# Kernel tuning notes

Hardware: AMD Instinct MI355X
Metric: run time of the kernel (lower is better)

## Reference

```python
import jax, jax.numpy as jnp
import numpy as np

B = 32768
T = 30
H = 384


def setup_inputs() -> dict:
    key = jax.random.key(0)
    ks = jax.random.split(key, 16)

    def lin(k, out_d, in_d):
        # torch nn.Linear init: U(-1/sqrt(in_d), 1/sqrt(in_d))
        bound = 1.0 / np.sqrt(in_d)
        kw, kb = jax.random.split(k)
        W = jax.random.uniform(kw, (out_d, in_d), jnp.float32, -bound, bound)
        b = jax.random.uniform(kb, (out_d,), jnp.float32, -bound, bound)
        return W, b

    Wp, bp = lin(ks[0], 128, 3)        # plan_input
    Ws, bs = lin(ks[1], 128, 3)        # state_input
    # GRUCell params: weight_ih [3H,128], weight_hh [3H,H], init U(-1/sqrt(H),..)
    gb = 1.0 / np.sqrt(H)
    W_ih = jax.random.uniform(ks[2], (3 * H, 128), jnp.float32, -gb, gb)
    b_ih = jax.random.uniform(ks[3], (3 * H,), jnp.float32, -gb, gb)
    W_hh = jax.random.uniform(ks[4], (3 * H, H), jnp.float32, -gb, gb)
    b_hh = jax.random.uniform(ks[5], (3 * H,), jnp.float32, -gb, gb)
    Wd1, bd1 = lin(ks[6], 64, H)       # decode Linear(384,64)
    Wd2, bd2 = lin(ks[7], 3, 64)       # decode Linear(64,3)

    init_hidden = jax.random.normal(ks[8], (B, H), jnp.float32)
    plan = jax.random.normal(ks[9], (B, T, 3), jnp.float32)
    gate = jax.random.uniform(ks[10], (B, 1), jnp.float32)
    init_state = jax.random.normal(ks[11], (B, 3), jnp.float32)

    return {
        "init_hidden": init_hidden, "plan": plan, "gate": gate,
        "init_state": init_state,
        "Wp": Wp, "bp": bp, "Ws": Ws, "bs": bs,
        "W_ih": W_ih, "b_ih": b_ih, "W_hh": W_hh, "b_hh": b_hh,
        "Wd1": Wd1, "bd1": bd1, "Wd2": Wd2, "bd2": bd2,
    }


def reference(init_hidden, plan, gate, init_state,
              Wp, bp, Ws, bs, W_ih, b_ih, W_hh, b_hh,
              Wd1, bd1, Wd2, bd2):
    # Dropout(0.1) is identity in eval mode.
    plan_seq = jnp.swapaxes(plan[:, :T, :3], 0, 1)  # [T,B,3]

    def step(carry, plan_t):
        hidden, state = carry  # [B,H], [B,3]
        x = (state @ Ws.T + bs) + (plan_t @ Wp.T + bp) * gate  # [B,128]
        gi = x @ W_ih.T + b_ih          # [B,3H]
        gh = hidden @ W_hh.T + b_hh     # [B,3H]
        ir, iz, inn = jnp.split(gi, 3, axis=-1)
        hr, hz, hn = jnp.split(gh, 3, axis=-1)
        r = jax.nn.sigmoid(ir + hr)
        z = jax.nn.sigmoid(iz + hz)
        n = jnp.tanh(inn + r * hn)
        hidden = (1.0 - z) * n + z * hidden
        dec = jax.nn.elu(hidden @ Wd1.T + bd1) @ Wd2.T + bd2  # [B,3]
        state = dec + state
        return (hidden, state), state

    _, outs = jax.lax.scan(step, (init_hidden, init_state[:, :3]), plan_seq)
    return jnp.swapaxes(outs, 0, 1)  # [B,T,3]
```

## Files before the change

kernel.cpp:

```cpp
#include <hip/hip_runtime.h>


#define TT  30
#define NPH 50
#define PHU 12288
#define HPU 6144
#define STRU 614400
#define HS  392

typedef unsigned short u16;
typedef __bf16 bf16x8 __attribute__((ext_vector_type(8)));
typedef u16    u16x8  __attribute__((ext_vector_type(8)));
typedef float  f32x16 __attribute__((ext_vector_type(16)));

__device__ __forceinline__ u16 f2b(float f){
  unsigned u = __float_as_uint(f);
  u += 0x7FFFu + ((u >> 16) & 1u);
  return (u16)(u >> 16);
}
__device__ __forceinline__ float b2f(u16 h){ return __uint_as_float(((unsigned)h) << 16); }

__device__ __forceinline__ f32x16 mfma32(u16x8 a, u16x8 b, f32x16 c){
  return __builtin_amdgcn_mfma_f32_32x32x16_bf16(
      __builtin_bit_cast(bf16x8, a), __builtin_bit_cast(bf16x8, b), c, 0, 0, 0);
}
__device__ __forceinline__ void lds_fence(){
  asm volatile("s_waitcnt lgkmcnt(0)" ::: "memory");
  __builtin_amdgcn_sched_barrier(0);
}
__device__ __forceinline__ float sigf(float x){ return __builtin_amdgcn_rcpf(1.f + __expf(-x)); }
__device__ __forceinline__ float tanh_(float x){ return 2.f*__builtin_amdgcn_rcpf(1.f + __expf(-2.f*x)) - 1.f; }

__device__ __forceinline__ void stage16(const u16* g, u16* l){
  __builtin_amdgcn_global_load_lds(
      (const __attribute__((address_space(1))) unsigned int*)g,
      (__attribute__((address_space(3))) unsigned int*)l, 16, 0, 0);
}

__global__ void prep_kernel(const float* __restrict__ Wih, const float* __restrict__ Whh,
                            const float* __restrict__ Wd1, const float* __restrict__ Wd2,
                            const float* __restrict__ bih, const float* __restrict__ bhh,
                            const float* __restrict__ Ws,  const float* __restrict__ bs,
                            const float* __restrict__ Wp,  const float* __restrict__ bp,
                            u16* __restrict__ stream, u16* __restrict__ wd2p,
                            u16* __restrict__ wxp, float* __restrict__ gb)
{
  int i = blockIdx.x*blockDim.x + threadIdx.x;
  if (i < 442368){
    int row = i/384, k = i - row*384;
    int g = row/384, unit = row - g*384, c = unit>>5, lc = unit&31;
    int kf = k>>4, hl = (k>>3)&1, j = k&7;
    int phase = c*4 + 1 + g;
    stream[(size_t)phase*PHU + kf*512 + (lc+32*hl)*8 + j] = f2b(Whh[i]);
  }
  if (i < 147456){
    int row = i>>7, k = i&127;
    int g = row/384, unit = row - g*384, c = unit>>5, lc = unit&31;
    int kf = k>>4, hl = (k>>3)&1, j = k&7;
    int phase = c*4;
    stream[(size_t)phase*PHU + (g*8+kf)*512 + (lc+32*hl)*8 + j] = f2b(Wih[i]);
  }
  if (i < 24576){
    int row = i/384, k = i - row*384;
    int ct = row>>5, lc = row&31;
    int kf = k>>4, hl = (k>>3)&1, j = k&7;
    int phase = 48 + ct;
    stream[(size_t)phase*PHU + kf*512 + (lc+32*hl)*8 + j] = f2b(Wd1[i]);
  }
  if (i < 2048){
    int kf = i>>9, r = i&511;
    int n = (r>>3)&31, hl = r>>8, j = r&7;
    int k = kf*16 + hl*8 + j;
    wd2p[i] = f2b((n<3) ? Wd2[n*64 + k] : 0.f);
  }
  if (i < 2048){
    int tl = i>>9, r = i&511;
    int n = (r>>3)&31, hl = r>>8, j = r&7;
    int k = hl*8 + j, u = tl*32 + n;
    float v = 0.f;
    if      (k <= 2) v = Ws[u*3 + k];
    else if (k == 3) v = bs[u];
    else if (k <= 6) v = Wp[u*3 + (k-4)];
    else if (k == 7) v = bp[u];
    wxp[i] = f2b(v);
  }
  if (i < 384){
    gb[i*4+0] = bih[i]       + bhh[i];
    gb[i*4+1] = bih[384+i]   + bhh[384+i];
    gb[i*4+2] = bih[768+i];
    gb[i*4+3] = bhh[768+i];
  }
}

#define PRELOAD(BN) { \
  const u16* W0_ = wb + ra*HPU + lane*8; \
  const u16* W1_ = wb + rb*HPU + lane*8; \
  _Pragma("unroll") for (int f_=0; f_<12; ++f_) BN[f_]    = *(const u16x8*)(W0_ + f_*512); \
  _Pragma("unroll") for (int f_=0; f_<12; ++f_) BN[12+f_] = *(const u16x8*)(W1_ + f_*512); }

#define PH_GH(ACC, BC, BN) { \
  stage_half(); stage_half(); \
  PRELOAD(BN); \
  _Pragma("unroll") for (int kf_=0; kf_<24; ++kf_) ACC = mfma32(hold[kf_], BC[kf_], ACC); \
  phase_end(); }

#define PH_GI(BC, BN) { \
  stage_half(); stage_half(); \
  PRELOAD(BN); \
  _Pragma("unroll") for (int kf_=0; kf_<8; ++kf_){ \
    aR  = mfma32(xf[kf_], BC[kf_],    aR); \
    aZ  = mfma32(xf[kf_], BC[8+kf_],  aZ); \
    aNI = mfma32(xf[kf_], BC[16+kf_], aNI); } \
  phase_end(); }

__global__ __launch_bounds__(256, 1)
void gru_main(const float* __restrict__ ih, const float* __restrict__ plan,
              const float* __restrict__ gate, const float* __restrict__ istate,
              const u16* __restrict__ stream, const u16* __restrict__ wd2p,
              const u16* __restrict__ wxp, const float* __restrict__ gb,
              const float* __restrict__ bd1, const float* __restrict__ bd2,
              float* __restrict__ out)
{
  __shared__ __attribute__((aligned(16))) u16 wb[5*HPU];
  __shared__ __attribute__((aligned(16))) u16 hn[4][32*HS];

  const int tid  = threadIdx.x;
  const int wave = tid >> 6, lane = tid & 63;
  const int m    = lane & 31, hl = lane >> 5;
  const int R0   = blockIdx.x*128 + wave*32;
  u16* hw = hn[wave];

  const float gt    = gate[R0 + m];
  const float bd1v0 = bd1[m], bd1v1 = bd1[32+m];
  const float bd2v  = (m<3) ? bd2[m] : 0.f;

  if (lane < 32){
    const float* sp = istate + (size_t)(R0+lane)*3;
    float* q = (float*)&hw[lane*HS + 384];
    q[0]=sp[0]; q[1]=sp[1]; q[2]=sp[2]; q[3]=0.f;
  }

  u16x8 hold[24];
#pragma unroll
  for (int kf=0; kf<24; ++kf){
    const float* p = ih + (size_t)(R0+m)*384 + kf*16 + hl*8;
    float4 a = *(const float4*)p;
    float4 b = *(const float4*)(p+4);
    u16x8 v;
    v[0]=f2b(a.x); v[1]=f2b(a.y); v[2]=f2b(a.z); v[3]=f2b(a.w);
    v[4]=f2b(b.x); v[5]=f2b(b.y); v[6]=f2b(b.z); v[7]=f2b(b.w);
    hold[kf]=v;
    *(u16x8*)&hw[m*HS + kf*16 + hl*8] = v;
  }

  int hoff = 0;
  int ss   = 0;
  int ra   = 0, rb = 1;
  auto stage_half = [&](){
    const u16* s = stream + hoff + wave*1536 + lane*8;
    u16* d = &wb[ss*HPU + wave*1536];
    stage16(s,        d);
    stage16(s + 512,  d + 512);
    stage16(s + 1024, d + 1024);
    hoff += HPU; if (hoff == STRU) hoff = 0;
    ss = (ss==4) ? 0 : ss+1;
  };
  auto phase_end = [&](){
    asm volatile("s_waitcnt vmcnt(3) lgkmcnt(0)" ::: "memory");
    __builtin_amdgcn_sched_barrier(0);
    __builtin_amdgcn_s_barrier();
    __builtin_amdgcn_sched_barrier(0);
    ra = (ra>=3) ? ra-3 : ra+2;
    rb = (rb>=3) ? rb-3 : rb+2;
  };

  u16x8 bfA[24], bfB[24];

  stage_half(); stage_half();
  asm volatile("s_waitcnt vmcnt(0)" ::: "memory");
  __builtin_amdgcn_sched_barrier(0);
  __builtin_amdgcn_s_barrier();
  __builtin_amdgcn_sched_barrier(0);
  PRELOAD(bfA);
  stage_half(); stage_half(); stage_half();
  asm volatile("s_waitcnt vmcnt(3) lgkmcnt(0)" ::: "memory");
  __builtin_amdgcn_sched_barrier(0);
  __builtin_amdgcn_s_barrier();
  __builtin_amdgcn_sched_barrier(0);
  ra = 2; rb = 3;

#pragma unroll 1
  for (int t=0; t<TT; ++t){
    u16x8 a8;
    {
      float4 sv = *(const float4*)&hw[m*HS + 384];
      const float* pp = plan + (size_t)(R0+m)*(TT*3) + t*3;
      float f0=sv.x, f1=sv.y, f2=sv.z, f3=1.f;
      float f4=gt*pp[0], f5=gt*pp[1], f6=gt*pp[2], f7=gt;
      if (hl){ a8[0]=0;a8[1]=0;a8[2]=0;a8[3]=0;a8[4]=0;a8[5]=0;a8[6]=0;a8[7]=0; }
      else { a8[0]=f2b(f0);a8[1]=f2b(f1);a8[2]=f2b(f2);a8[3]=f2b(f3);
             a8[4]=f2b(f4);a8[5]=f2b(f5);a8[6]=f2b(f6);a8[7]=f2b(f7); }
    }
    u16x8 xf[8];
#pragma unroll
    for (int tl=0; tl<4; ++tl){
      f32x16 ax;
#pragma unroll
      for (int r=0;r<16;++r) ax[r]=0.f;
      ax = mfma32(a8, *(const u16x8*)(wxp + tl*512 + lane*8), ax);
#pragma unroll
      for (int r=0;r<16;++r){
        int row = (r&3) + ((r>>2)<<3) + 4*hl;
        hw[row*HS + m] = f2b(ax[r]);
      }
      lds_fence();
      xf[2*tl]   = *(const u16x8*)&hw[m*HS + hl*8];
      xf[2*tl+1] = *(const u16x8*)&hw[m*HS + 16 + hl*8];
      lds_fence();
    }
    *(u16x8*)&hw[m*HS + hl*8]      = hold[0];
    *(u16x8*)&hw[m*HS + 16 + hl*8] = hold[1];
    lds_fence();

#pragma unroll 1
    for (int c=0; c<12; ++c){
      f32x16 aR, aZ, aNI, aNH;
      {
        const float4 b4 = *(const float4*)(gb + (size_t)(c*32+m)*4);
#pragma unroll
        for (int r=0;r<16;++r){ aR[r]=b4.x; aZ[r]=b4.y; aNI[r]=b4.z; aNH[r]=b4.w; }
      }
      PH_GI(bfA, bfB);
      PH_GH(aR, bfB, bfA);
      PH_GH(aZ, bfA, bfB);
      {
        stage_half(); stage_half();
        PRELOAD(bfA);
#pragma unroll
        for (int kf=0; kf<24; ++kf)
          aNH = mfma32(hold[kf], bfB[kf], aNH);
#pragma unroll
        for (int r=0;r<16;++r){
          int row = (r&3) + ((r>>2)<<3) + 4*hl;
          float rr = sigf(aR[r]);
          float zz = sigf(aZ[r]);
          float nn = tanh_(aNI[r] + rr*aNH[r]);
          int off = row*HS + c*32 + m;
          float ho = b2f(hw[off]);
          hw[off] = f2b((1.f-zz)*nn + zz*ho);
        }
        phase_end();
      }
    }

    lds_fence();
#pragma unroll
    for (int kf=0; kf<24; ++kf)
      hold[kf] = *(const u16x8*)&hw[m*HS + kf*16 + hl*8];

    f32x16 a0, a1;
#pragma unroll
    for (int r=0;r<16;++r){ a0[r]=bd1v0; a1[r]=bd1v1; }
    PH_GH(a0, bfA, bfB);
    {
      stage_half(); stage_half();
      PRELOAD(bfA);
#pragma unroll
      for (int kf=0; kf<24; ++kf)
        a1 = mfma32(hold[kf], bfB[kf], a1);

      u16x8 wd2f0 = *(const u16x8*)(wd2p + 0*512 + lane*8);
      u16x8 wd2f1 = *(const u16x8*)(wd2p + 1*512 + lane*8);
      u16x8 wd2f2 = *(const u16x8*)(wd2p + 2*512 + lane*8);
      u16x8 wd2f3 = *(const u16x8*)(wd2p + 3*512 + lane*8);

      f32x16 ao;
#pragma unroll
      for (int r=0;r<16;++r) ao[r]=0.f;
#pragma unroll
      for (int r=0;r<16;++r){
        int row = (r&3) + ((r>>2)<<3) + 4*hl;
        float e = a0[r]; e = e>0.f ? e : (__expf(e)-1.f);
        hw[row*HS + m] = f2b(e);
      }
      lds_fence();
      {
        u16x8 af0 = *(const u16x8*)&hw[m*HS + hl*8];
        u16x8 af1 = *(const u16x8*)&hw[m*HS + 16 + hl*8];
        ao = mfma32(af0, wd2f0, ao);
        ao = mfma32(af1, wd2f1, ao);
      }
      lds_fence();
#pragma unroll
      for (int r=0;r<16;++r){
        int row = (r&3) + ((r>>2)<<3) + 4*hl;
        float e = a1[r]; e = e>0.f ? e : (__expf(e)-1.f);
        hw[row*HS + m] = f2b(e);
      }
      lds_fence();
      {
        u16x8 af0 = *(const u16x8*)&hw[m*HS + hl*8];
        u16x8 af1 = *(const u16x8*)&hw[m*HS + 16 + hl*8];
        ao = mfma32(af0, wd2f2, ao);
        ao = mfma32(af1, wd2f3, ao);
      }
      lds_fence();
      *(u16x8*)&hw[m*HS + hl*8]      = hold[0];
      *(u16x8*)&hw[m*HS + 16 + hl*8] = hold[1];

#pragma unroll
      for (int r=0;r<16;++r){
        int row = (r&3) + ((r>>2)<<3) + 4*hl;
        if (m < 3){
          float* q = (float*)&hw[row*HS + 384];
          float ns = q[m] + ao[r] + bd2v;
          out[(size_t)(R0+row)*(TT*3) + t*3 + m] = ns;
          q[m] = ns;
        }
      }
      phase_end();
    }
  }
}

extern "C" void kernel_launch(void* const* d_in, const int* in_sizes, int n_in,
                              void* d_out, int out_size, void* d_ws, size_t ws_size,
                              hipStream_t stream)
{
  (void)in_sizes; (void)n_in; (void)out_size; (void)ws_size;
  const float* ih     = (const float*)d_in[0];
  const float* plan   = (const float*)d_in[1];
  const float* gatep  = (const float*)d_in[2];
  const float* istate = (const float*)d_in[3];
  const float* Wp     = (const float*)d_in[4];
  const float* bp     = (const float*)d_in[5];
  const float* Ws     = (const float*)d_in[6];
  const float* bs     = (const float*)d_in[7];
  const float* Wih    = (const float*)d_in[8];
  const float* bih    = (const float*)d_in[9];
  const float* Whh    = (const float*)d_in[10];
  const float* bhh    = (const float*)d_in[11];
  const float* Wd1    = (const float*)d_in[12];
  const float* bd1    = (const float*)d_in[13];
  const float* Wd2    = (const float*)d_in[14];
  const float* bd2    = (const float*)d_in[15];

  u16*   wstream = (u16*)d_ws;
  u16*   wd2p    = (u16*)((char*)d_ws + 1228800);
  u16*   wxp     = (u16*)((char*)d_ws + 1232896);
  float* gb      = (float*)((char*)d_ws + 1236992);

  prep_kernel<<<1728, 256, 0, stream>>>(Wih, Whh, Wd1, Wd2, bih, bhh, Ws, bs, Wp, bp,
                                        wstream, wd2p, wxp, gb);
  gru_main<<<256, 256, 0, stream>>>(ih, plan, gatep, istate,
                                    wstream, wd2p, wxp, gb, bd1, bd2, (float*)d_out);
}
```

Measured before the change: 1.645 ms.

## Stream GRU weights directly from global/L2 into registers, dropping LDS staging

Replaces the cooperative global_load_lds staging of weight halves into a shared ring buffer, and its per-phase waitcnt and s_barrier, with per-wave direct global loads into register double buffers (bfA/bfB) that are issued in the middle of each phase's MFMA chain. The intent is to remove most block-wide barriers and the LDS round trip, so the four waves run independently and weight fetches overlap with compute. In exchange, every wave now fetches the full weight stream from L2 itself, which multiplies cache traffic by four. The prefetch distance is also only half a phase, so load latency may be exposed. One barrier per timestep is kept.

```diff
diff --git a/kernel.cpp b/kernel.cpp
--- a/kernel.cpp
+++ b/kernel.cpp
@@ -2,10 +2,8 @@
 
 
 #define TT  30
-#define NPH 50
 #define PHU 12288
 #define HPU 6144
-#define STRU 614400
 #define HS  392
 
 typedef unsigned short u16;
@@ -30,12 +28,6 @@
 }
 __device__ __forceinline__ float sigf(float x){ return __builtin_amdgcn_rcpf(1.f + __expf(-x)); }
 __device__ __forceinline__ float tanh_(float x){ return 2.f*__builtin_amdgcn_rcpf(1.f + __expf(-2.f*x)) - 1.f; }
-
-__device__ __forceinline__ void stage16(const u16* g, u16* l){
-  __builtin_amdgcn_global_load_lds(
-      (const __attribute__((address_space(1))) unsigned int*)g,
-      (__attribute__((address_space(3))) unsigned int*)l, 16, 0, 0);
-}
 
 __global__ void prep_kernel(const float* __restrict__ Wih, const float* __restrict__ Whh,
                             const float* __restrict__ Wd1, const float* __restrict__ Wd2,
@@ -92,26 +84,24 @@
   }
 }
 
-#define PRELOAD(BN) { \
-  const u16* W0_ = wb + ra*HPU + lane*8; \
-  const u16* W1_ = wb + rb*HPU + lane*8; \
-  _Pragma("unroll") for (int f_=0; f_<12; ++f_) BN[f_]    = *(const u16x8*)(W0_ + f_*512); \
-  _Pragma("unroll") for (int f_=0; f_<12; ++f_) BN[12+f_] = *(const u16x8*)(W1_ + f_*512); }
-
-#define PH_GH(ACC, BC, BN) { \
-  stage_half(); stage_half(); \
-  PRELOAD(BN); \
-  _Pragma("unroll") for (int kf_=0; kf_<24; ++kf_) ACC = mfma32(hold[kf_], BC[kf_], ACC); \
-  phase_end(); }
-
-#define PH_GI(BC, BN) { \
-  stage_half(); stage_half(); \
-  PRELOAD(BN); \
-  _Pragma("unroll") for (int kf_=0; kf_<8; ++kf_){ \
-    aR  = mfma32(xf[kf_], BC[kf_],    aR); \
-    aZ  = mfma32(xf[kf_], BC[8+kf_],  aZ); \
-    aNI = mfma32(xf[kf_], BC[16+kf_], aNI); } \
-  phase_end(); }
+#define LOAD_HALF(BN) { \
+  const u16* s_ = stream + (size_t)nh*HPU + lane*8; \
+  _Pragma("unroll") for (int f_=0; f_<12; ++f_) BN[f_] = *(const u16x8*)(s_ + f_*512); \
+  nh = (nh==99) ? 0 : nh+1; }
+
+#define PH_GI() { \
+  _Pragma("unroll") for (int q_=0;q_<8;++q_) aR  = mfma32(xf[q_],   bfA[q_],   aR); \
+  _Pragma("unroll") for (int q_=0;q_<4;++q_) aZ  = mfma32(xf[q_],   bfA[8+q_], aZ); \
+  LOAD_HALF(bfA); \
+  _Pragma("unroll") for (int q_=0;q_<4;++q_) aZ  = mfma32(xf[4+q_], bfB[q_],   aZ); \
+  _Pragma("unroll") for (int q_=0;q_<8;++q_) aNI = mfma32(xf[q_],   bfB[4+q_], aNI); \
+  LOAD_HALF(bfB); }
+
+#define PH_GH(ACC) { \
+  _Pragma("unroll") for (int k_=0;k_<12;++k_) ACC = mfma32(hold[k_],    bfA[k_], ACC); \
+  LOAD_HALF(bfA); \
+  _Pragma("unroll") for (int k_=0;k_<12;++k_) ACC = mfma32(hold[12+k_], bfB[k_], ACC); \
+  LOAD_HALF(bfB); }
 
 __global__ __launch_bounds__(256, 1)
 void gru_main(const float* __restrict__ ih, const float* __restrict__ plan,
@@ -121,7 +111,6 @@
               const float* __restrict__ bd1, const float* __restrict__ bd2,
               float* __restrict__ out)
 {
-  __shared__ __attribute__((aligned(16))) u16 wb[5*HPU];
   __shared__ __attribute__((aligned(16))) u16 hn[4][32*HS];
 
   const int tid  = threadIdx.x;
@@ -153,44 +142,15 @@
     *(u16x8*)&hw[m*HS + kf*16 + hl*8] = v;
   }
 
-  int hoff = 0;
-  int ss   = 0;
-  int ra   = 0, rb = 1;
-  auto stage_half = [&](){
-    const u16* s = stream + hoff + wave*1536 + lane*8;
-    u16* d = &wb[ss*HPU + wave*1536];
-    stage16(s,        d);
-    stage16(s + 512,  d + 512);
-    stage16(s + 1024, d + 1024);
-    hoff += HPU; if (hoff == STRU) hoff = 0;
-    ss = (ss==4) ? 0 : ss+1;
-  };
-  auto phase_end = [&](){
-    asm volatile("s_waitcnt vmcnt(3) lgkmcnt(0)" ::: "memory");
-    __builtin_amdgcn_sched_barrier(0);
-    __builtin_amdgcn_s_barrier();
-    __builtin_amdgcn_sched_barrier(0);
-    ra = (ra>=3) ? ra-3 : ra+2;
-    rb = (rb>=3) ? rb-3 : rb+2;
-  };
-
-  u16x8 bfA[24], bfB[24];
-
-  stage_half(); stage_half();
-  asm volatile("s_waitcnt vmcnt(0)" ::: "memory");
-  __builtin_amdgcn_sched_barrier(0);
-  __builtin_amdgcn_s_barrier();
-  __builtin_amdgcn_sched_barrier(0);
-  PRELOAD(bfA);
-  stage_half(); stage_half(); stage_half();
-  asm volatile("s_waitcnt vmcnt(3) lgkmcnt(0)" ::: "memory");
-  __builtin_amdgcn_sched_barrier(0);
-  __builtin_amdgcn_s_barrier();
-  __builtin_amdgcn_sched_barrier(0);
-  ra = 2; rb = 3;
+  u16x8 bfA[12], bfB[12];
+  int nh = 0;
+  LOAD_HALF(bfA);
+  LOAD_HALF(bfB);
 
 #pragma unroll 1
   for (int t=0; t<TT; ++t){
+    __builtin_amdgcn_s_barrier();
+
     u16x8 a8;
     {
       float4 sv = *(const float4*)&hw[m*HS + 384];
@@ -230,26 +190,19 @@
 #pragma unroll
         for (int r=0;r<16;++r){ aR[r]=b4.x; aZ[r]=b4.y; aNI[r]=b4.z; aNH[r]=b4.w; }
       }
-      PH_GI(bfA, bfB);
-      PH_GH(aR, bfB, bfA);
-      PH_GH(aZ, bfA, bfB);
-      {
-        stage_half(); stage_half();
-        PRELOAD(bfA);
-#pragma unroll
-        for (int kf=0; kf<24; ++kf)
-          aNH = mfma32(hold[kf], bfB[kf], aNH);
-#pragma unroll
-        for (int r=0;r<16;++r){
-          int row = (r&3) + ((r>>2)<<3) + 4*hl;
-          float rr = sigf(aR[r]);
-          float zz = sigf(aZ[r]);
-          float nn = tanh_(aNI[r] + rr*aNH[r]);
-          int off = row*HS + c*32 + m;
-          float ho = b2f(hw[off]);
-          hw[off] = f2b((1.f-zz)*nn + zz*ho);
-        }
-        phase_end();
+      PH_GI();
+      PH_GH(aR);
+      PH_GH(aZ);
+      PH_GH(aNH);
+#pragma unroll
+      for (int r=0;r<16;++r){
+        int row = (r&3) + ((r>>2)<<3) + 4*hl;
+        float rr = sigf(aR[r]);
+        float zz = sigf(aZ[r]);
+        float nn = tanh_(aNI[r] + rr*aNH[r]);
+        int off = row*HS + c*32 + m;
+        float ho = b2f(hw[off]);
+        hw[off] = f2b((1.f-zz)*nn + zz*ho);
       }
     }
 
@@ -261,14 +214,9 @@
     f32x16 a0, a1;
 #pragma unroll
     for (int r=0;r<16;++r){ a0[r]=bd1v0; a1[r]=bd1v1; }
-    PH_GH(a0, bfA, bfB);
+    PH_GH(a0);
+    PH_GH(a1);
     {
-      stage_half(); stage_half();
-      PRELOAD(bfA);
-#pragma unroll
-      for (int kf=0; kf<24; ++kf)
-        a1 = mfma32(hold[kf], bfB[kf], a1);
-
       u16x8 wd2f0 = *(const u16x8*)(wd2p + 0*512 + lane*8);
       u16x8 wd2f1 = *(const u16x8*)(wd2p + 1*512 + lane*8);
       u16x8 wd2f2 = *(const u16x8*)(wd2p + 2*512 + lane*8);
@@ -318,7 +266,6 @@
           q[m] = ns;
         }
       }
-      phase_end();
     }
   }
 }
```

New measurement: 2.001 ms. 21.7% more time.

## Halve weight register double-buffer by loading LDS weight halves mid-phase

Applied to the files above, without the earlier changes.

Replaces the full 24-fragment double-buffered weight registers with two 12-fragment halves. Each phase now loads the second half from LDS while the first half's MFMAs run, then prefetches the next phase's first half before the remaining MFMAs. The aim is to cut VGPR pressure and the chance of spilling, while keeping LDS-to-register loads overlapped with MFMA work. In exchange, LDS load latency sits closer to its consumers inside each phase, and the prologue and slot-index rotation change.

```diff
diff --git a/kernel.cpp b/kernel.cpp
--- a/kernel.cpp
+++ b/kernel.cpp
@@ -92,25 +92,26 @@
   }
 }
 
-#define PRELOAD(BN) { \
-  const u16* W0_ = wb + ra*HPU + lane*8; \
-  const u16* W1_ = wb + rb*HPU + lane*8; \
-  _Pragma("unroll") for (int f_=0; f_<12; ++f_) BN[f_]    = *(const u16x8*)(W0_ + f_*512); \
-  _Pragma("unroll") for (int f_=0; f_<12; ++f_) BN[12+f_] = *(const u16x8*)(W1_ + f_*512); }
-
-#define PH_GH(ACC, BC, BN) { \
+#define LOADHALF(BN, S) { \
+  const u16* W_ = wb + (S)*HPU + lane*8; \
+  _Pragma("unroll") for (int f_=0; f_<12; ++f_) BN[f_] = *(const u16x8*)(W_ + f_*512); }
+
+#define PH_GH(ACC) { \
+  LOADHALF(bfB, s1); \
+  _Pragma("unroll") for (int k_=0;k_<12;++k_) ACC = mfma32(hold[k_], bfA[k_], ACC); \
+  LOADHALF(bfA, s2); \
   stage_half(); stage_half(); \
-  PRELOAD(BN); \
-  _Pragma("unroll") for (int kf_=0; kf_<24; ++kf_) ACC = mfma32(hold[kf_], BC[kf_], ACC); \
+  _Pragma("unroll") for (int k_=0;k_<12;++k_) ACC = mfma32(hold[12+k_], bfB[k_], ACC); \
   phase_end(); }
 
-#define PH_GI(BC, BN) { \
+#define PH_GI() { \
+  LOADHALF(bfB, s1); \
+  _Pragma("unroll") for (int q_=0;q_<8;++q_) aR = mfma32(xf[q_], bfA[q_],   aR); \
+  _Pragma("unroll") for (int q_=0;q_<4;++q_) aZ = mfma32(xf[q_], bfA[8+q_], aZ); \
+  LOADHALF(bfA, s2); \
   stage_half(); stage_half(); \
-  PRELOAD(BN); \
-  _Pragma("unroll") for (int kf_=0; kf_<8; ++kf_){ \
-    aR  = mfma32(xf[kf_], BC[kf_],    aR); \
-    aZ  = mfma32(xf[kf_], BC[8+kf_],  aZ); \
-    aNI = mfma32(xf[kf_], BC[16+kf_], aNI); } \
+  _Pragma("unroll") for (int q_=0;q_<4;++q_) aZ  = mfma32(xf[4+q_], bfB[q_],   aZ); \
+  _Pragma("unroll") for (int q_=0;q_<8;++q_) aNI = mfma32(xf[q_],   bfB[4+q_], aNI); \
   phase_end(); }
 
 __global__ __launch_bounds__(256, 1)
@@ -155,7 +156,7 @@
 
   int hoff = 0;
   int ss   = 0;
-  int ra   = 0, rb = 1;
+  int s1   = 1, s2 = 2;
   auto stage_half = [&](){
     const u16* s = stream + hoff + wave*1536 + lane*8;
     u16* d = &wb[ss*HPU + wave*1536];
@@ -170,24 +171,21 @@
     __builtin_amdgcn_sched_barrier(0);
     __builtin_amdgcn_s_barrier();
     __builtin_amdgcn_sched_barrier(0);
-    ra = (ra>=3) ? ra-3 : ra+2;
-    rb = (rb>=3) ? rb-3 : rb+2;
+    s1 = (s1>=3) ? s1-3 : s1+2;
+    s2 = (s2>=3) ? s2-3 : s2+2;
   };
 
-  u16x8 bfA[24], bfB[24];
-
-  stage_half(); stage_half();
-  asm volatile("s_waitcnt vmcnt(0)" ::: "memory");
+  u16x8 bfA[12], bfB[12];
+
+  stage_half(); stage_half(); stage_half(); stage_half();
+  asm volatile("s_waitcnt vmcnt(3)" ::: "memory");
   __builtin_amdgcn_sched_barrier(0);
   __builtin_amdgcn_s_barrier();
   __builtin_amdgcn_sched_barrier(0);
-  PRELOAD(bfA);
-  stage_half(); stage_half(); stage_half();
-  asm volatile("s_waitcnt vmcnt(3) lgkmcnt(0)" ::: "memory");
-  __builtin_amdgcn_sched_barrier(0);
+  LOADHALF(bfA, 0);
+  lds_fence();
   __builtin_amdgcn_s_barrier();
   __builtin_amdgcn_sched_barrier(0);
-  ra = 2; rb = 3;
 
 #pragma unroll 1
   for (int t=0; t<TT; ++t){
@@ -230,15 +228,19 @@
 #pragma unroll
         for (int r=0;r<16;++r){ aR[r]=b4.x; aZ[r]=b4.y; aNI[r]=b4.z; aNH[r]=b4.w; }
       }
-      PH_GI(bfA, bfB);
-      PH_GH(aR, bfB, bfA);
-      PH_GH(aZ, bfA, bfB);
+      PH_GI();
+      PH_GH(aR);
+      PH_GH(aZ);
       {
+        LOADHALF(bfB, s1);
+#pragma unroll
+        for (int kf=0; kf<12; ++kf)
+          aNH = mfma32(hold[kf], bfA[kf], aNH);
+        LOADHALF(bfA, s2);
         stage_half(); stage_half();
-        PRELOAD(bfA);
-#pragma unroll
-        for (int kf=0; kf<24; ++kf)
-          aNH = mfma32(hold[kf], bfB[kf], aNH);
+#pragma unroll
+        for (int kf=0; kf<12; ++kf)
+          aNH = mfma32(hold[12+kf], bfB[kf], aNH);
 #pragma unroll
         for (int r=0;r<16;++r){
           int row = (r&3) + ((r>>2)<<3) + 4*hl;
@@ -261,13 +263,17 @@
     f32x16 a0, a1;
 #pragma unroll
     for (int r=0;r<16;++r){ a0[r]=bd1v0; a1[r]=bd1v1; }
-    PH_GH(a0, bfA, bfB);
+    PH_GH(a0);
     {
+      LOADHALF(bfB, s1);
+#pragma unroll
+      for (int kf=0; kf<12; ++kf)
+        a1 = mfma32(hold[kf], bfA[kf], a1);
+      LOADHALF(bfA, s2);
       stage_half(); stage_half();
-      PRELOAD(bfA);
-#pragma unroll
-      for (int kf=0; kf<24; ++kf)
-        a1 = mfma32(hold[kf], bfB[kf], a1);
+#pragma unroll
+      for (int kf=0; kf<12; ++kf)
+        a1 = mfma32(hold[12+kf], bfB[kf], a1);
 
       u16x8 wd2f0 = *(const u16x8*)(wd2p + 0*512 + lane*8);
       u16x8 wd2f1 = *(const u16x8*)(wd2p + 1*512 + lane*8);
```

After: 1.524 ms. -7.4%, faster.
